# Performance work log

Hardware: AMD Instinct MI355X
Metric: run time of the kernel (lower is better)

The kernel has to match this reference:

```python
import jax, jax.numpy as jnp
import numpy as np

MARGIN = 0.3
EPS = 1e-6  # torch pairwise_distance default eps used by TripletMarginLoss


def setup_inputs() -> dict:
    key = jax.random.key(0)
    k1, k2 = jax.random.split(key)
    emb = jax.random.normal(k1, (4096, 256), dtype=jnp.float32)
    emb = emb / jnp.linalg.norm(emb, axis=1, keepdims=True)  # docstring: normalized embeddings
    labels = jax.random.randint(k2, (4096,), 0, 64, dtype=jnp.int64) if jax.config.jax_enable_x64 else jax.random.randint(k2, (4096,), 0, 64, dtype=jnp.int32)
    return {"embeddings": emb, "labels": labels}


def _triplet_mining_loss(embeddings, labels):
    B = embeddings.shape[0]
    # pairwise euclidean distances via GEMM (matches torch.cdist p=2)
    sq = jnp.sum(embeddings * embeddings, axis=1)
    d2 = sq[:, None] + sq[None, :] - 2.0 * (embeddings @ embeddings.T)
    dist = jnp.sqrt(jnp.maximum(d2, 0.0))  # [B, B]

    same = labels[:, None] == labels[None, :]
    eye = jnp.eye(B, dtype=bool)
    pos_mask = same & ~eye
    neg_mask = ~same
    valid = pos_mask.any(axis=1) & neg_mask.any(axis=1)

    # hardest positive per anchor
    ap = jnp.where(pos_mask, dist, -jnp.inf)
    hp_idx = jnp.argmax(ap, axis=1)                           # [B]
    ap_dist = jnp.take_along_axis(dist, hp_idx[:, None], 1)[:, 0]

    # semi-hard negative: ap < d_an < ap + margin; pick FIRST such index (original takes semi_hard_indices[0])
    semi = neg_mask & (dist > ap_dist[:, None]) & (dist < ap_dist[:, None] + MARGIN)
    any_semi = semi.any(axis=1)
    first_semi = jnp.argmax(semi, axis=1)                     # argmax of bool = first True
    an = jnp.where(neg_mask, dist, jnp.inf)
    hardest_neg = jnp.argmin(an, axis=1)
    neg_idx = jnp.where(any_semi, first_semi, hardest_neg)

    # triplet margin loss recomputed from embeddings (torch adds EPS inside the norm)
    pos_e = embeddings[hp_idx]
    neg_e = embeddings[neg_idx]
    d_ap = jnp.linalg.norm(embeddings - pos_e + EPS, axis=1)
    d_an = jnp.linalg.norm(embeddings - neg_e + EPS, axis=1)
    per_anchor = jnp.maximum(d_ap - d_an + MARGIN, 0.0)

    vf = valid.astype(embeddings.dtype)
    cnt = jnp.sum(vf)
    return jnp.where(cnt > 0, jnp.sum(per_anchor * vf) / jnp.maximum(cnt, 1.0), 0.0)


def reference(embeddings, labels):
    return _triplet_mining_loss(embeddings, labels)
```

## Files before the change

### kernel.cpp

```cpp
#include <hip/hip_runtime.h>
#include <math.h>

#define BN 4096
#define DIM 256
#define D4 (DIM/4)
#define MI 8
#define MT 16
#define MARGINF 0.3f
#define EPSF 1e-6f
#define SCAP 96
#define IMAX 0x7fffffff

typedef __attribute__((ext_vector_type(8))) short bf16x8;
typedef __attribute__((ext_vector_type(4))) float f32x4;

__device__ __forceinline__ float fma4(float4 a, float4 b, float c){
  return fmaf(a.x,b.x, fmaf(a.y,b.y, fmaf(a.z,b.z, fmaf(a.w,b.w, c))));
}
__device__ __forceinline__ unsigned short f2bf(float x){
  unsigned u = __float_as_uint(x);
  return (unsigned short)((u + 0x7FFFu + ((u>>16)&1u)) >> 16);
}
__device__ __forceinline__ float bf2f(unsigned short h){
  return __uint_as_float(((unsigned)h)<<16);
}

__global__ __launch_bounds__(256) void k_pre2(const float* __restrict__ E,
     unsigned short* __restrict__ EhiT, unsigned short* __restrict__ EloT,
     float* __restrict__ sq, unsigned int* __restrict__ counter){
  int t = threadIdx.x;
  int b = blockIdx.x;
  const float4* E4 = (const float4*)E;
  bf16x8* HT = (bf16x8*)EhiT;
  bf16x8* LT = (bf16x8*)EloT;
  #pragma unroll
  for (int it=0; it<8; it++){
    int g  = b*4 + (it>>1);
    int kk = (it&1)*4 + (t>>6);
    int sub = t&63, q = sub>>4, n = sub&15;
    int r = g*16 + n;
    int c = kk*4 + q;
    float4 v0 = E4[(size_t)r*64 + c*2];
    float4 v1 = E4[(size_t)r*64 + c*2 + 1];
    unsigned short h[8], lo[8];
    float vv[8] = {v0.x,v0.y,v0.z,v0.w, v1.x,v1.y,v1.z,v1.w};
    #pragma unroll
    for (int i=0;i<8;i++){ h[i]=f2bf(vv[i]); lo[i]=f2bf(vv[i]-bf2f(h[i])); }
    bf16x8 hv, lv;
    #pragma unroll
    for (int i=0;i<8;i++){ hv[i]=(short)h[i]; lv[i]=(short)lo[i]; }
    size_t d = (size_t)g*512 + (size_t)kk*64 + sub;
    HT[d] = hv; LT[d] = lv;
  }
  int row = t>>2, part = t&3;
  const float4* rp = E4 + (size_t)(b*64+row)*D4 + part*16;
  float s0=0.f, s1=0.f;
  #pragma unroll
  for (int i=0;i<16;i+=2){ s0=fma4(rp[i],rp[i],s0); s1=fma4(rp[i+1],rp[i+1],s1); }
  float s = s0+s1;
  s += __shfl_xor(s,1); s += __shfl_xor(s,2);
  if (part==0) sq[b*64+row] = s;
  if (b==0 && t==0) counter[0] = 0u;
}

__global__ __launch_bounds__(1024,4) void k_main_m(const float* __restrict__ E,
     const unsigned short* __restrict__ EhiT, const unsigned short* __restrict__ EloT,
     const int* __restrict__ labels, const float* __restrict__ sq,
     float* __restrict__ partials, unsigned int* __restrict__ counter, float* __restrict__ out){
  __shared__ int   labsS[BN];
  __shared__ float sqS[BN];
  __shared__ bf16x8 afH[512];
  __shared__ bf16x8 afL[512];
  __shared__ float rnv[16][MT]; __shared__ int rnj[16][MT]; __shared__ int rsm[16][MT];
  __shared__ float apS[MT]; __shared__ int hpS[MT]; __shared__ int posOk[MT];
  __shared__ int finNeg[MT]; __shared__ int finVal[MT];
  __shared__ float lossS[MT];
  __shared__ float rs[16], rc[16];
  __shared__ int lastFlag;
  int t=threadIdx.x, l=t&63, w=t>>6;
  int lane16 = l&15, quad = l>>4;
  int a0 = blockIdx.x * MT;
  const bf16x8* HT = (const bf16x8*)EhiT;
  const bf16x8* LT = (const bf16x8*)EloT;
  const float4* E4 = (const float4*)E;
  size_t ABase = (size_t)blockIdx.x * 512;

  ((int4*)labsS)[t]  = ((const int4*)labels)[t];
  ((float4*)sqS)[t]  = ((const float4*)sq)[t];
  if (t < 512){ afH[t] = HT[ABase + t]; afL[t] = LT[ABase + t]; }
  __syncthreads();
  float sqa[4]; int laba[4];
  #pragma unroll
  for (int r=0;r<4;r++){ sqa[r]=sqS[a0+quad*4+r]; laba[r]=labsS[a0+quad*4+r]; }

  {
    int aw = a0 + w;
    int labW = labsS[aw];
    float sqw_ = sqS[aw];
    float4 areg = E4[(size_t)aw*64 + l];
    float bv2 = -INFINITY; int bj = IMAX;
    for (int c=0; c<64; c++){
      bool m = (labsS[c*64 + l] == labW);
      unsigned long long mask = __ballot(m);
      while (mask){
        int b = __ffsll((unsigned long long)mask) - 1;
        mask &= mask - 1ull;
        int j = c*64 + b;
        if (j == aw) continue;
        float4 bjv = E4[(size_t)j*64 + l];
        float p = fma4(areg, bjv, 0.0f);
        #pragma unroll
        for (int off=32; off; off>>=1) p += __shfl_xor(p, off);
        float d2 = sqw_ + sqS[j] - 2.0f*p;
        if (d2 > bv2){ bv2 = d2; bj = j; }
      }
    }
    if (l==0){
      posOk[w] = (bj != IMAX);
      apS[w] = (bj==IMAX) ? -INFINITY : sqrtf(fmaxf(bv2, 0.0f));
      hpS[w] = (bj==IMAX) ? 0 : bj;
    }
  }
  __syncthreads();

  {
    float ap2[4], th2[4];
    #pragma unroll
    for (int r=0;r<4;r++){
      float ap = apS[quad*4+r];
      ap2[r] = ap*ap;
      float th = ap + MARGINF;
      th2[r] = th*th;
    }
    float mn[4]; int mj[4]; int sm[4];
    #pragma unroll
    for (int r=0;r<4;r++){ mn[r]=INFINITY; mj[r]=IMAX; sm[r]=IMAX; }
    #pragma unroll 1
    for (int tile=0; tile<16; tile++){
      int gb = w*16 + tile;
      size_t BBase = (size_t)gb * 512;
      f32x4 acc0={0.f,0.f,0.f,0.f}, acc1={0.f,0.f,0.f,0.f}, acc2={0.f,0.f,0.f,0.f};
      #pragma unroll 2
      for (int kk=0; kk<8; kk++){
        bf16x8 ah = afH[kk*64 + l];
        bf16x8 al = afL[kk*64 + l];
        bf16x8 bh = HT[BBase + kk*64 + l];
        bf16x8 bl = LT[BBase + kk*64 + l];
        acc0 = __builtin_amdgcn_mfma_f32_16x16x32_bf16(ah, bh, acc0, 0,0,0);
        acc1 = __builtin_amdgcn_mfma_f32_16x16x32_bf16(ah, bl, acc1, 0,0,0);
        acc2 = __builtin_amdgcn_mfma_f32_16x16x32_bf16(al, bh, acc2, 0,0,0);
      }
      int j = gb*16 + lane16;
      int lj = labsS[j]; float sqj = sqS[j];
      #pragma unroll
      for (int r=0;r<4;r++){
        float dot = acc0[r] + (acc1[r] + acc2[r]);
        float d2v = sqa[r] + sqj - 2.0f*dot;
        if (lj != laba[r]){
          if (d2v < mn[r]){ mn[r]=d2v; mj[r]=j; }
          if (d2v > ap2[r] && d2v < th2[r] && j < sm[r]) sm[r]=j;
        }
      }
    }
    #pragma unroll
    for (int r=0;r<4;r++){
      float v=mn[r]; int j=mj[r]; int s=sm[r];
      #pragma unroll
      for (int off=1; off<16; off<<=1){
        float v2=__shfl_xor(v,off); int j2=__shfl_xor(j,off); int s2=__shfl_xor(s,off);
        if (v2<v || (v2==v && j2<j)){ v=v2; j=j2; }
        s = (s2<s)?s2:s;
      }
      if (lane16==0){ rnv[w][quad*4+r]=v; rnj[w][quad*4+r]=j; rsm[w][quad*4+r]=s; }
    }
  }
  __syncthreads();
  if (t < MT){
    int a=t;
    float V=INFINITY; int J=IMAX; int S=IMAX;
    for (int q=0;q<16;q++){
      float v2=rnv[q][a]; int j2=rnj[q][a];
      if (v2<V || (v2==V && j2<J)){ V=v2; J=j2; }
      int s2=rsm[q][a]; S=(s2<S)?s2:S;
    }
    bool anyneg = (J != IMAX);
    int ng = (S != IMAX) ? S : J;
    finNeg[a] = (ng==IMAX) ? 0 : ng;
    finVal[a] = (posOk[a] && anyneg) ? 1 : 0;
  }
  __syncthreads();

  {
    int a = w;
    float sp=0.f, sn=0.f;
    int dov = finVal[a];
    if (dov){
      int hp = hpS[a], ng = finNeg[a];
      float4 av = E4[(size_t)(a0+a)*64 + l];
      float4 pv = E4[(size_t)hp*64 + l];
      float4 nv = E4[(size_t)ng*64 + l];
      float d0=av.x-pv.x+EPSF, d1=av.y-pv.y+EPSF, d2=av.z-pv.z+EPSF, d3=av.w-pv.w+EPSF;
      sp = fmaf(d0,d0, fmaf(d1,d1, fmaf(d2,d2, d3*d3)));
      float n0=av.x-nv.x+EPSF, n1=av.y-nv.y+EPSF, n2=av.z-nv.z+EPSF, n3=av.w-nv.w+EPSF;
      sn = fmaf(n0,n0, fmaf(n1,n1, fmaf(n2,n2, n3*n3)));
    }
    #pragma unroll
    for (int off=32; off; off>>=1){ sp += __shfl_xor(sp,off); sn += __shfl_xor(sn,off); }
    if (l==0) lossS[a] = dov ? fmaxf(sqrtf(sp)-sqrtf(sn)+MARGINF, 0.0f) : 0.0f;
  }
  __syncthreads();

  if (t==0){
    float lsum=0.f, lcnt=0.f;
    for (int a=0;a<MT;a++){ lsum += lossS[a]; lcnt += (float)finVal[a]; }
    partials[2*blockIdx.x]   = lsum;
    partials[2*blockIdx.x+1] = lcnt;
    __threadfence();
    unsigned int old = atomicAdd(counter, 1u);
    lastFlag = (old == gridDim.x - 1) ? 1 : 0;
  }
  __syncthreads();
  if (lastFlag){
    __threadfence();
    float s=0.f, c=0.f;
    if (t < 256){ s = partials[2*t]; c = partials[2*t+1]; }
    #pragma unroll
    for (int off=32; off; off>>=1){ s += __shfl_xor(s,off); c += __shfl_xor(c,off); }
    if (l==0){ rs[w]=s; rc[w]=c; }
    __syncthreads();
    if (t==0){
      float S=0.f, C=0.f;
      for (int q=0;q<16;q++){ S+=rs[q]; C+=rc[q]; }
      out[0] = (C>0.0f) ? S/fmaxf(C,1.0f) : 0.0f;
    }
  }
}

__global__ __launch_bounds__(256) void k_sq(const float* __restrict__ E, float* __restrict__ sq){
  int i = blockIdx.x*256 + threadIdx.x;
  if (i >= BN) return;
  const float4* r = (const float4*)E + (size_t)i*D4;
  float a0=0.f,a1=0.f,a2=0.f,a3=0.f;
  #pragma unroll
  for (int q=0;q<D4;q+=4){
    a0 = fma4(r[q],r[q],a0);   a1 = fma4(r[q+1],r[q+1],a1);
    a2 = fma4(r[q+2],r[q+2],a2); a3 = fma4(r[q+3],r[q+3],a3);
  }
  sq[i] = (a0+a1)+(a2+a3);
}

__global__ __launch_bounds__(256) void k_pos(const float* __restrict__ E, const int* __restrict__ labels,
                       const float* __restrict__ sq, float* __restrict__ apw,
                       int* __restrict__ hpw, int* __restrict__ anypw){
  __shared__ int members[1024];
  __shared__ float4 mem4[SCAP*65];
  __shared__ int cnts[16][4];
  __shared__ int offs[16][4];
  __shared__ int cntS;
  int t = threadIdx.x, lane = t&63, w = t>>6;
  int c = blockIdx.x >> 2, split = blockIdx.x & 3;
  for (int ch=0; ch<16; ch++){
    bool m = (labels[ch*256 + t] == c);
    unsigned long long mask = __ballot(m);
    if (lane==0) cnts[ch][w] = __popcll(mask);
  }
  __syncthreads();
  if (t==0){
    int run=0;
    for (int ch=0; ch<16; ch++)
      for (int q=0;q<4;q++){ offs[ch][q]=run; run+=cnts[ch][q]; }
    cntS = run;
  }
  __syncthreads();
  int cnt = cntS; if (cnt>1024) cnt=1024;
  for (int ch=0; ch<16; ch++){
    int idx = ch*256 + t;
    bool m = (labels[idx] == c);
    unsigned long long mask = __ballot(m);
    int my = __popcll(mask & ((1ull<<lane)-1ull));
    int pos = offs[ch][w] + my;
    if (m && pos < 1024) members[pos] = idx;
  }
  int S = (cnt < SCAP) ? cnt : SCAP;
  int anyp = (cnt >= 2) ? 1 : 0;
  __syncthreads();
  const float4* E4 = (const float4*)E;
  for (int idx=t; idx<S*64; idx+=256){
    int row = idx>>6, f = idx&63;
    mem4[row*65 + f] = E4[(size_t)members[row]*D4 + f];
  }
  __syncthreads();
  int esplit = split*4 + w;
  int p = lane&3, cand = lane>>2;
  int passes = (cnt+15)>>4;
  for (int mi=esplit; mi<cnt; mi+=16){
    int i = members[mi];
    float sqi = sq[i];
    float4 ai4[16];
    if (mi < S){
      #pragma unroll
      for (int m=0;m<16;m++) ai4[m] = mem4[mi*65 + p + 4*m];
    } else {
      #pragma unroll
      for (int m=0;m<16;m++) ai4[m] = E4[(size_t)i*D4 + p + 4*m];
    }
    float bv = -INFINITY; int bj = IMAX;
    for (int ps=0; ps<passes; ps++){
      int mj = ps*16 + cand;
      if (mj < cnt && mj != mi){
        int j = members[mj];
        float a0v=0.f, a1v=0.f;
        if (mj < S){
          const float4* rj = mem4 + mj*65 + p;
          #pragma unroll
          for (int m=0;m<16;m+=2){ a0v=fma4(ai4[m],rj[4*m],a0v); a1v=fma4(ai4[m+1],rj[4*(m+1)],a1v); }
        } else {
          const float4* rj = E4 + (size_t)j*D4 + p;
          #pragma unroll
          for (int m=0;m<16;m+=2){ a0v=fma4(ai4[m],rj[4*m],a0v); a1v=fma4(ai4[m+1],rj[4*(m+1)],a1v); }
        }
        float acc = a0v+a1v;
        acc += __shfl_xor(acc,1); acc += __shfl_xor(acc,2);
        float d = sqrtf(fmaxf(sqi + sq[j] - 2.0f*acc, 0.0f));
        if (p==0){ if (d > bv || (d==bv && j<bj)){ bv=d; bj=j; } }
      }
    }
    #pragma unroll
    for (int off=32; off; off>>=1){
      float v2=__shfl_xor(bv,off); int j2=__shfl_xor(bj,off);
      if (v2>bv || (v2==bv && j2<bj)){ bv=v2; bj=j2; }
    }
    if (lane==0){
      int J = (bj==IMAX) ? 0 : bj;
      apw[i]=bv; hpw[i]=J; anypw[i]=anyp;
    }
  }
}

__global__ __launch_bounds__(256,2) void k_main(const float* __restrict__ E, const int* __restrict__ labels,
     const float* __restrict__ sq, const float* __restrict__ apw, const int* __restrict__ hpw,
     const int* __restrict__ anypw, float* __restrict__ partials){
  __shared__ float4 At[MI*68 + 4];
  __shared__ float redv[4][MI]; __shared__ int redj[4][MI]; __shared__ int redsm[4][MI];
  __shared__ int finNeg[MI]; __shared__ int finVal[MI];
  __shared__ float redp[4], redn[4];
  int t=threadIdx.x, lane=t&63, w=t>>6;
  int a0 = blockIdx.x * MI;
  const float4* E4 = (const float4*)E;
  for (int idx=t; idx<MI*64; idx+=256){
    int a=idx>>6, q=idx&63, pp=q&3, mm=q>>2;
    At[a*68 + pp*17 + mm] = E4[(size_t)(a0+a)*D4 + q];
  }
  __syncthreads();
  float apv[MI], sqi[MI]; int labi[MI];
  #pragma unroll
  for (int a=0;a<MI;a++){ apv[a]=apw[a0+a]; sqi[a]=sq[a0+a]; labi[a]=labels[a0+a]; }
  float mnv[MI]; int mnj[MI]; int smj[MI];
  #pragma unroll
  for (int a=0;a<MI;a++){ mnv[a]=INFINITY; mnj[a]=0; smj[a]=IMAX; }
  int s = t>>2, p = t&3;
  for (int it=0; it<16; it++){
    int colb = it*256 + 4*s;
    const float4* __restrict__ bp = E4 + (size_t)colb*D4 + p;
    float acc[MI][4];
    #pragma unroll
    for (int a=0;a<MI;a++){
      #pragma unroll
      for (int c2=0;c2<4;c2++) acc[a][c2]=0.0f;
    }
    for (int mg=0; mg<4; mg++){
      float4 b[4][4];
      #pragma unroll
      for (int c2=0;c2<4;c2++){
        #pragma unroll
        for (int m=0;m<4;m++) b[m][c2] = bp[(size_t)c2*D4 + mg*16 + m*4];
      }
      #pragma unroll
      for (int a=0;a<MI;a++){
        float4 a4[4];
        #pragma unroll
        for (int m=0;m<4;m++) a4[m] = At[a*68 + p*17 + mg*4 + m];
        #pragma unroll
        for (int m=0;m<4;m++){
          #pragma unroll
          for (int c2=0;c2<4;c2++) acc[a][c2] = fma4(a4[m], b[m][c2], acc[a][c2]);
        }
      }
    }
    #pragma unroll
    for (int a=0;a<MI;a++){
      #pragma unroll
      for (int c2=0;c2<4;c2++){
        float v = acc[a][c2];
        v += __shfl_xor(v,1); v += __shfl_xor(v,2);
        acc[a][c2] = v;
      }
    }
    #pragma unroll
    for (int c2=0;c2<4;c2++){
      int j = colb + c2;
      int lj = labels[j]; float sqj = sq[j];
      #pragma unroll
      for (int a=0;a<MI;a++){
        float d = sqrtf(fmaxf(sqi[a]+sqj-2.0f*acc[a][c2], 0.0f));
        if (lj != labi[a]){
          if (d < mnv[a]){ mnv[a]=d; mnj[a]=j; }
          if (d > apv[a] && d < apv[a]+MARGINF && j < smj[a]) smj[a]=j;
        }
      }
    }
  }
  #pragma unroll
  for (int a=0;a<MI;a++){
    float v=mnv[a]; int j=mnj[a]; int sm=smj[a];
    #pragma unroll
    for (int off=32; off; off>>=1){
      float v2=__shfl_xor(v,off); int j2=__shfl_xor(j,off); int s2=__shfl_xor(sm,off);
      if (v2<v || (v2==v && j2<j)){ v=v2; j=j2; }
      sm = (s2<sm)?s2:sm;
    }
    if (lane==0){ redv[w][a]=v; redj[w][a]=j; redsm[w][a]=sm; }
  }
  __syncthreads();
  if (t < MI){
    int a=t;
    float V=INFINITY; int J=0; int S=IMAX; bool first=true;
    for (int q=0;q<4;q++){
      float v2=redv[q][a]; int j2=redj[q][a];
      if (first || v2<V || (v2==V && j2<J)){ V=v2; J=j2; first=false; }
      int s2=redsm[q][a]; S=(s2<S)?s2:S;
    }
    bool anyneg = (V < INFINITY);
    finNeg[a] = (S != IMAX) ? S : J;
    finVal[a] = (anypw[a0+a] != 0 && anyneg) ? 1 : 0;
  }
  __syncthreads();
  float lsum=0.0f, lcnt=0.0f;
  for (int a=0;a<MI;a++){
    if (finVal[a]){
      int hp = hpw[a0+a]; int ng = finNeg[a];
      float ai = E[(size_t)(a0+a)*DIM + t];
      float pv = E[(size_t)hp*DIM + t];
      float nv = E[(size_t)ng*DIM + t];
      float dp = ai - pv + EPSF; float dn = ai - nv + EPSF;
      float sp = dp*dp, sn = dn*dn;
      #pragma unroll
      for (int off=32; off; off>>=1){ sp += __shfl_xor(sp,off); sn += __shfl_xor(sn,off); }
      if (lane==0){ redp[w]=sp; redn[w]=sn; }
    }
    __syncthreads();
    if (finVal[a] && t==0){
      float SP=(redp[0]+redp[1])+(redp[2]+redp[3]);
      float SN=(redn[0]+redn[1])+(redn[2]+redn[3]);
      lsum += fmaxf(sqrtf(SP)-sqrtf(SN)+MARGINF, 0.0f);
      lcnt += 1.0f;
    }
    __syncthreads();
  }
  if (t==0){ partials[2*blockIdx.x]=lsum; partials[2*blockIdx.x+1]=lcnt; }
}

__global__ __launch_bounds__(256) void k_fin(const float* __restrict__ partials, float* __restrict__ out, int nb){
  __shared__ float rs[4], rc[4];
  int t=threadIdx.x, lane=t&63, w=t>>6;
  float s=0.f, c=0.f;
  for (int q=t;q<nb;q+=256){ s+=partials[2*q]; c+=partials[2*q+1]; }
  #pragma unroll
  for (int off=32; off; off>>=1){ s+=__shfl_xor(s,off); c+=__shfl_xor(c,off); }
  if (lane==0){ rs[w]=s; rc[w]=c; }
  __syncthreads();
  if (t==0){
    float S=(rs[0]+rs[1])+(rs[2]+rs[3]);
    float C=(rc[0]+rc[1])+(rc[2]+rc[3]);
    out[0] = (C>0.0f) ? S/fmaxf(C,1.0f) : 0.0f;
  }
}

extern "C" void kernel_launch(void* const* d_in, const int* in_sizes, int n_in,
                              void* d_out, int out_size, void* d_ws, size_t ws_size,
                              hipStream_t stream) {
  const float* E      = (const float*)d_in[0];
  const int*   labels = (const int*)d_in[1];
  float* out = (float*)d_out;

  float* sqw      = (float*)d_ws;
  float* apw      = sqw + BN;
  int*   hpw      = (int*)(apw + BN);
  int*   anypw    = hpw + BN;
  float* partials = (float*)(anypw + BN);
  unsigned int* counter = (unsigned int*)(partials + 1024);
  unsigned short* EhiT = (unsigned short*)((char*)d_ws + 131072);
  unsigned short* EloT = EhiT + (size_t)BN*DIM;
  bool big = ws_size >= (size_t)(131072 + 4*1024*1024);

  if (big){
    k_pre2  <<<64,    256,  0, stream>>>(E, EhiT, EloT, sqw, counter);
    k_main_m<<<BN/MT, 1024, 0, stream>>>(E, EhiT, EloT, labels, sqw, partials, counter, out);
  } else {
    k_sq  <<<BN/256, 256, 0, stream>>>(E, sqw);
    k_pos <<<256,    256, 0, stream>>>(E, labels, sqw, apw, hpw, anypw);
    k_main<<<BN/MI,  256, 0, stream>>>(E, labels, sqw, apw, hpw, anypw, partials);
    k_fin <<<1,      256, 0, stream>>>(partials, out, BN/MI);
  }
}
```

Measured before the change: 156.0 us.

## Split fused triplet kernel into positive, negative-mining and finalize stages

Replaces the single fused kernel with separate stages. A positive-mining kernel compacts same-label candidates into shared memory and computes four dot products per loop iteration. A negative-mining MFMA kernel processes 32 anchors per block over half of the candidate columns, reusing each B tile across two anchor groups, and merges the halves through 64-bit atomicMin keys. A small finalize kernel then computes the loss. This is meant to remove the serial per-anchor positive search from the MFMA kernel and raise parallelism and data reuse, at the cost of more launches, atomics and global round-trips. The positive candidate list is capped at 512 entries.

```diff
diff --git a/kernel.cpp b/kernel.cpp
--- a/kernel.cpp
+++ b/kernel.cpp
@@ -5,11 +5,11 @@
 #define DIM 256
 #define D4 (DIM/4)
 #define MI 8
-#define MT 16
 #define MARGINF 0.3f
 #define EPSF 1e-6f
 #define SCAP 96
 #define IMAX 0x7fffffff
+#define PCAP 512
 
 typedef __attribute__((ext_vector_type(8))) short bf16x8;
 typedef __attribute__((ext_vector_type(4))) float f32x4;
@@ -29,15 +29,14 @@
      unsigned short* __restrict__ EhiT, unsigned short* __restrict__ EloT,
      float* __restrict__ sq, unsigned int* __restrict__ counter){
   int t = threadIdx.x;
-  int b = blockIdx.x;
+  int g = blockIdx.x;
   const float4* E4 = (const float4*)E;
   bf16x8* HT = (bf16x8*)EhiT;
   bf16x8* LT = (bf16x8*)EloT;
   #pragma unroll
-  for (int it=0; it<8; it++){
-    int g  = b*4 + (it>>1);
-    int kk = (it&1)*4 + (t>>6);
-    int sub = t&63, q = sub>>4, n = sub&15;
+  for (int it=0; it<2; it++){
+    int idx = it*256 + t;
+    int kk = idx>>6, sub = idx&63, q = sub>>4, n = sub&15;
     int r = g*16 + n;
     int c = kk*4 + q;
     float4 v0 = E4[(size_t)r*64 + c*2];
@@ -49,172 +48,242 @@
     bf16x8 hv, lv;
     #pragma unroll
     for (int i=0;i<8;i++){ hv[i]=(short)h[i]; lv[i]=(short)lo[i]; }
-    size_t d = (size_t)g*512 + (size_t)kk*64 + sub;
+    size_t d = (size_t)g*512 + idx;
     HT[d] = hv; LT[d] = lv;
   }
-  int row = t>>2, part = t&3;
-  const float4* rp = E4 + (size_t)(b*64+row)*D4 + part*16;
-  float s0=0.f, s1=0.f;
-  #pragma unroll
-  for (int i=0;i<16;i+=2){ s0=fma4(rp[i],rp[i],s0); s1=fma4(rp[i+1],rp[i+1],s1); }
+  int row = t>>4, part = t&15;
+  const float4* rp = E4 + (size_t)(g*16+row)*64 + part*4;
+  float s0 = fma4(rp[0],rp[0],0.f);
+  float s1 = fma4(rp[1],rp[1],0.f);
+  s0 = fma4(rp[2],rp[2],s0);
+  s1 = fma4(rp[3],rp[3],s1);
   float s = s0+s1;
-  s += __shfl_xor(s,1); s += __shfl_xor(s,2);
-  if (part==0) sq[b*64+row] = s;
-  if (b==0 && t==0) counter[0] = 0u;
-}
-
-__global__ __launch_bounds__(1024,4) void k_main_m(const float* __restrict__ E,
+  s += __shfl_xor(s,1); s += __shfl_xor(s,2); s += __shfl_xor(s,4); s += __shfl_xor(s,8);
+  if (part==0) sq[g*16+row] = s;
+  if (g==0 && t==0) counter[0] = 0u;
+}
+
+__global__ __launch_bounds__(256) void k_posm(const float* __restrict__ E,
+     const int* __restrict__ labels, const float* __restrict__ sq,
+     float* __restrict__ apw, int* __restrict__ hpw,
+     unsigned long long* __restrict__ negKey, unsigned int* __restrict__ semiJ){
+  __shared__ __align__(16) int   labsS[BN];
+  __shared__ __align__(16) float sqS[BN];
+  __shared__ int mem[4][PCAP+4];
+  int t=threadIdx.x, l=t&63, w=t>>6;
+  #pragma unroll
+  for (int i=0;i<4;i++){
+    ((int4*)labsS)[i*256+t]   = ((const int4*)labels)[i*256+t];
+    ((float4*)sqS)[i*256+t]   = ((const float4*)sq)[i*256+t];
+  }
+  __syncthreads();
+  int aw = blockIdx.x*4 + w;
+  int labW = labsS[aw];
+  float sqw_ = sqS[aw];
+  const float4* E4 = (const float4*)E;
+  float4 areg = E4[(size_t)aw*64 + l];
+  int cnt = 0;
+  for (int c=0;c<64;c++){
+    int j = c*64 + l;
+    bool m = (labsS[j]==labW) && (j != aw);
+    unsigned long long mask = __ballot(m);
+    if (m){
+      int pos = cnt + __popcll(mask & ((1ull<<l)-1ull));
+      if (pos < PCAP) mem[w][pos] = j;
+    }
+    cnt += __popcll(mask);
+  }
+  if (cnt > PCAP) cnt = PCAP;
+  if (l < 4) mem[w][cnt + l] = aw;
+  float bv2 = -INFINITY; int bj = IMAX;
+  for (int base=0; base<cnt; base+=4){
+    int j0=mem[w][base+0], j1=mem[w][base+1], j2=mem[w][base+2], j3=mem[w][base+3];
+    float4 r0=E4[(size_t)j0*64+l];
+    float4 r1=E4[(size_t)j1*64+l];
+    float4 r2=E4[(size_t)j2*64+l];
+    float4 r3=E4[(size_t)j3*64+l];
+    float p0=fma4(areg,r0,0.f), p1=fma4(areg,r1,0.f);
+    float p2=fma4(areg,r2,0.f), p3=fma4(areg,r3,0.f);
+    #pragma unroll
+    for (int off=32; off; off>>=1){
+      p0 += __shfl_xor(p0,off); p1 += __shfl_xor(p1,off);
+      p2 += __shfl_xor(p2,off); p3 += __shfl_xor(p3,off);
+    }
+    float d0 = sqw_ + sqS[j0] - 2.0f*p0;
+    float d1 = sqw_ + sqS[j1] - 2.0f*p1;
+    float d2 = sqw_ + sqS[j2] - 2.0f*p2;
+    float d3 = sqw_ + sqS[j3] - 2.0f*p3;
+    if (d0 > bv2){ bv2=d0; bj=j0; }
+    if (base+1<cnt && d1 > bv2){ bv2=d1; bj=j1; }
+    if (base+2<cnt && d2 > bv2){ bv2=d2; bj=j2; }
+    if (base+3<cnt && d3 > bv2){ bv2=d3; bj=j3; }
+  }
+  if (l==0){
+    apw[aw] = (bj==IMAX) ? -INFINITY : sqrtf(fmaxf(bv2, 0.0f));
+    hpw[aw] = (bj==IMAX) ? 0 : bj;
+    negKey[aw] = ~0ull;
+    semiJ[aw]  = 0xFFFFFFFFu;
+  }
+}
+
+__global__ __launch_bounds__(1024,4) void k_negm(
      const unsigned short* __restrict__ EhiT, const unsigned short* __restrict__ EloT,
      const int* __restrict__ labels, const float* __restrict__ sq,
-     float* __restrict__ partials, unsigned int* __restrict__ counter, float* __restrict__ out){
-  __shared__ int   labsS[BN];
-  __shared__ float sqS[BN];
-  __shared__ bf16x8 afH[512];
-  __shared__ bf16x8 afL[512];
-  __shared__ float rnv[16][MT]; __shared__ int rnj[16][MT]; __shared__ int rsm[16][MT];
-  __shared__ float apS[MT]; __shared__ int hpS[MT]; __shared__ int posOk[MT];
-  __shared__ int finNeg[MT]; __shared__ int finVal[MT];
-  __shared__ float lossS[MT];
-  __shared__ float rs[16], rc[16];
-  __shared__ int lastFlag;
+     const float* __restrict__ apw,
+     unsigned long long* __restrict__ negKey, unsigned int* __restrict__ semiJ){
+  __shared__ bf16x8 afH[1024];
+  __shared__ bf16x8 afL[1024];
+  __shared__ __align__(16) int   labsH[2048];
+  __shared__ __align__(16) float sqH[2048];
+  __shared__ float rnv[16][32]; __shared__ int rnj[16][32]; __shared__ int rsm[16][32];
   int t=threadIdx.x, l=t&63, w=t>>6;
   int lane16 = l&15, quad = l>>4;
-  int a0 = blockIdx.x * MT;
+  int q8   = blockIdx.x & 7;
+  int half = q8 >> 2;
+  int grp  = (blockIdx.x >> 3)*4 + (q8 & 3);
+  int a0 = grp*32;
+  int hbase = half*2048;
   const bf16x8* HT = (const bf16x8*)EhiT;
   const bf16x8* LT = (const bf16x8*)EloT;
-  const float4* E4 = (const float4*)E;
-  size_t ABase = (size_t)blockIdx.x * 512;
-
-  ((int4*)labsS)[t]  = ((const int4*)labels)[t];
-  ((float4*)sqS)[t]  = ((const float4*)sq)[t];
-  if (t < 512){ afH[t] = HT[ABase + t]; afL[t] = LT[ABase + t]; }
-  __syncthreads();
-  float sqa[4]; int laba[4];
-  #pragma unroll
-  for (int r=0;r<4;r++){ sqa[r]=sqS[a0+quad*4+r]; laba[r]=labsS[a0+quad*4+r]; }
-
-  {
-    int aw = a0 + w;
-    int labW = labsS[aw];
-    float sqw_ = sqS[aw];
-    float4 areg = E4[(size_t)aw*64 + l];
-    float bv2 = -INFINITY; int bj = IMAX;
-    for (int c=0; c<64; c++){
-      bool m = (labsS[c*64 + l] == labW);
-      unsigned long long mask = __ballot(m);
-      while (mask){
-        int b = __ffsll((unsigned long long)mask) - 1;
-        mask &= mask - 1ull;
-        int j = c*64 + b;
-        if (j == aw) continue;
-        float4 bjv = E4[(size_t)j*64 + l];
-        float p = fma4(areg, bjv, 0.0f);
-        #pragma unroll
-        for (int off=32; off; off>>=1) p += __shfl_xor(p, off);
-        float d2 = sqw_ + sqS[j] - 2.0f*p;
-        if (d2 > bv2){ bv2 = d2; bj = j; }
-      }
-    }
-    if (l==0){
-      posOk[w] = (bj != IMAX);
-      apS[w] = (bj==IMAX) ? -INFINITY : sqrtf(fmaxf(bv2, 0.0f));
-      hpS[w] = (bj==IMAX) ? 0 : bj;
-    }
-  }
-  __syncthreads();
-
-  {
-    float ap2[4], th2[4];
-    #pragma unroll
-    for (int r=0;r<4;r++){
-      float ap = apS[quad*4+r];
-      ap2[r] = ap*ap;
+  afH[t] = HT[(size_t)grp*1024 + t];
+  afL[t] = LT[(size_t)grp*1024 + t];
+  { int2   lv = ((const int2*)(labels + hbase))[t];
+    labsH[2*t] = lv.x; labsH[2*t+1] = lv.y;
+    float2 sv = ((const float2*)(sq + hbase))[t];
+    sqH[2*t] = sv.x; sqH[2*t+1] = sv.y; }
+  float sqa[2][4]; int laba[2][4]; float ap2[2][4]; float th2[2][4];
+  #pragma unroll
+  for (int g=0; g<2; g++){
+    #pragma unroll
+    for (int r=0; r<4; r++){
+      int ag = a0 + g*16 + quad*4 + r;
+      sqa[g][r] = sq[ag]; laba[g][r] = labels[ag];
+      float ap = apw[ag];
+      ap2[g][r] = ap*ap;
       float th = ap + MARGINF;
-      th2[r] = th*th;
-    }
-    float mn[4]; int mj[4]; int sm[4];
-    #pragma unroll
-    for (int r=0;r<4;r++){ mn[r]=INFINITY; mj[r]=IMAX; sm[r]=IMAX; }
-    #pragma unroll 1
-    for (int tile=0; tile<16; tile++){
-      int gb = w*16 + tile;
-      size_t BBase = (size_t)gb * 512;
-      f32x4 acc0={0.f,0.f,0.f,0.f}, acc1={0.f,0.f,0.f,0.f}, acc2={0.f,0.f,0.f,0.f};
-      #pragma unroll 2
-      for (int kk=0; kk<8; kk++){
-        bf16x8 ah = afH[kk*64 + l];
-        bf16x8 al = afL[kk*64 + l];
-        bf16x8 bh = HT[BBase + kk*64 + l];
-        bf16x8 bl = LT[BBase + kk*64 + l];
-        acc0 = __builtin_amdgcn_mfma_f32_16x16x32_bf16(ah, bh, acc0, 0,0,0);
-        acc1 = __builtin_amdgcn_mfma_f32_16x16x32_bf16(ah, bl, acc1, 0,0,0);
-        acc2 = __builtin_amdgcn_mfma_f32_16x16x32_bf16(al, bh, acc2, 0,0,0);
-      }
-      int j = gb*16 + lane16;
-      int lj = labsS[j]; float sqj = sqS[j];
-      #pragma unroll
-      for (int r=0;r<4;r++){
-        float dot = acc0[r] + (acc1[r] + acc2[r]);
-        float d2v = sqa[r] + sqj - 2.0f*dot;
-        if (lj != laba[r]){
-          if (d2v < mn[r]){ mn[r]=d2v; mj[r]=j; }
-          if (d2v > ap2[r] && d2v < th2[r] && j < sm[r]) sm[r]=j;
-        }
-      }
-    }
-    #pragma unroll
-    for (int r=0;r<4;r++){
-      float v=mn[r]; int j=mj[r]; int s=sm[r];
+      th2[g][r] = th*th;
+    }
+  }
+  __syncthreads();
+  float mn[2][4]; int mj[2][4]; int sm[2][4];
+  #pragma unroll
+  for (int g=0; g<2; g++)
+    #pragma unroll
+    for (int r=0; r<4; r++){ mn[g][r]=INFINITY; mj[g][r]=IMAX; sm[g][r]=IMAX; }
+  #pragma unroll 1
+  for (int tile=0; tile<8; tile++){
+    int gl = w*8 + tile;
+    size_t BBase = (size_t)(half*128 + gl) * 512;
+    f32x4 acc00={0.f,0.f,0.f,0.f}, acc01=acc00, acc02=acc00;
+    f32x4 acc10=acc00, acc11=acc00, acc12=acc00;
+    #pragma unroll 2
+    for (int kk=0; kk<8; kk++){
+      bf16x8 bh  = HT[BBase + kk*64 + l];
+      bf16x8 bl  = LT[BBase + kk*64 + l];
+      bf16x8 ah0 = afH[kk*64 + l];
+      bf16x8 al0 = afL[kk*64 + l];
+      bf16x8 ah1 = afH[512 + kk*64 + l];
+      bf16x8 al1 = afL[512 + kk*64 + l];
+      acc00 = __builtin_amdgcn_mfma_f32_16x16x32_bf16(ah0, bh, acc00, 0,0,0);
+      acc01 = __builtin_amdgcn_mfma_f32_16x16x32_bf16(ah0, bl, acc01, 0,0,0);
+      acc02 = __builtin_amdgcn_mfma_f32_16x16x32_bf16(al0, bh, acc02, 0,0,0);
+      acc10 = __builtin_amdgcn_mfma_f32_16x16x32_bf16(ah1, bh, acc10, 0,0,0);
+      acc11 = __builtin_amdgcn_mfma_f32_16x16x32_bf16(ah1, bl, acc11, 0,0,0);
+      acc12 = __builtin_amdgcn_mfma_f32_16x16x32_bf16(al1, bh, acc12, 0,0,0);
+    }
+    int jloc = gl*16 + lane16;
+    int lj = labsH[jloc]; float sqj = sqH[jloc];
+    int jglob = hbase + jloc;
+    #pragma unroll
+    for (int r=0; r<4; r++){
+      float dot0 = acc00[r] + (acc01[r] + acc02[r]);
+      float d20  = sqa[0][r] + sqj - 2.0f*dot0;
+      if (lj != laba[0][r]){
+        if (d20 < mn[0][r]){ mn[0][r]=d20; mj[0][r]=jglob; }
+        if (d20 > ap2[0][r] && d20 < th2[0][r] && jglob < sm[0][r]) sm[0][r]=jglob;
+      }
+      float dot1 = acc10[r] + (acc11[r] + acc12[r]);
+      float d21  = sqa[1][r] + sqj - 2.0f*dot1;
+      if (lj != laba[1][r]){
+        if (d21 < mn[1][r]){ mn[1][r]=d21; mj[1][r]=jglob; }
+        if (d21 > ap2[1][r] && d21 < th2[1][r] && jglob < sm[1][r]) sm[1][r]=jglob;
+      }
+    }
+  }
+  #pragma unroll
+  for (int g=0; g<2; g++){
+    #pragma unroll
+    for (int r=0; r<4; r++){
+      float v=mn[g][r]; int j=mj[g][r]; int s=sm[g][r];
       #pragma unroll
       for (int off=1; off<16; off<<=1){
         float v2=__shfl_xor(v,off); int j2=__shfl_xor(j,off); int s2=__shfl_xor(s,off);
         if (v2<v || (v2==v && j2<j)){ v=v2; j=j2; }
         s = (s2<s)?s2:s;
       }
-      if (lane16==0){ rnv[w][quad*4+r]=v; rnj[w][quad*4+r]=j; rsm[w][quad*4+r]=s; }
-    }
-  }
-  __syncthreads();
-  if (t < MT){
-    int a=t;
+      if (lane16==0){
+        int ai = g*16 + quad*4 + r;
+        rnv[w][ai]=v; rnj[w][ai]=j; rsm[w][ai]=s;
+      }
+    }
+  }
+  __syncthreads();
+  if (t < 32){
     float V=INFINITY; int J=IMAX; int S=IMAX;
-    for (int q=0;q<16;q++){
-      float v2=rnv[q][a]; int j2=rnj[q][a];
+    for (int q=0; q<16; q++){
+      float v2=rnv[q][t]; int j2=rnj[q][t];
       if (v2<V || (v2==V && j2<J)){ V=v2; J=j2; }
-      int s2=rsm[q][a]; S=(s2<S)?s2:S;
-    }
-    bool anyneg = (J != IMAX);
-    int ng = (S != IMAX) ? S : J;
-    finNeg[a] = (ng==IMAX) ? 0 : ng;
-    finVal[a] = (posOk[a] && anyneg) ? 1 : 0;
-  }
-  __syncthreads();
-
-  {
-    int a = w;
-    float sp=0.f, sn=0.f;
-    int dov = finVal[a];
+      int s2=rsm[q][t]; S=(s2<S)?s2:S;
+    }
+    unsigned u = __float_as_uint(V);
+    unsigned key = (u & 0x80000000u) ? ~u : (u | 0x80000000u);
+    unsigned long long k64 = (((unsigned long long)key)<<32) | (unsigned)J;
+    atomicMin(&negKey[a0+t], k64);
+    if (S != IMAX) atomicMin(&semiJ[a0+t], (unsigned)S);
+  }
+}
+
+__global__ __launch_bounds__(256) void k_fin2(const float* __restrict__ E,
+     const float* __restrict__ apw, const int* __restrict__ hpw,
+     const unsigned long long* __restrict__ negKey, const unsigned int* __restrict__ semiJ,
+     float* __restrict__ partials, unsigned int* __restrict__ counter,
+     float* __restrict__ out){
+  __shared__ float lsumS[4], lcntS[4];
+  __shared__ float rs[4], rc[4];
+  __shared__ int lastFlag;
+  int t=threadIdx.x, l=t&63, w=t>>6;
+  const float4* E4 = (const float4*)E;
+  float lsum=0.f, lcnt=0.f;
+  #pragma unroll 1
+  for (int i=0;i<4;i++){
+    int a = blockIdx.x*16 + w*4 + i;
+    unsigned long long k64 = negKey[a];
+    unsigned Jn = (unsigned)(k64 & 0xFFFFFFFFull);
+    unsigned Sn = semiJ[a];
+    bool anyneg = (Jn != (unsigned)IMAX);
+    int ng = (Sn != 0xFFFFFFFFu) ? (int)Sn : (int)Jn;
+    float ap = apw[a];
+    bool dov = (ap != -INFINITY) && anyneg;
     if (dov){
-      int hp = hpS[a], ng = finNeg[a];
-      float4 av = E4[(size_t)(a0+a)*64 + l];
+      int hp = hpw[a];
+      float4 av = E4[(size_t)a*64 + l];
       float4 pv = E4[(size_t)hp*64 + l];
       float4 nv = E4[(size_t)ng*64 + l];
       float d0=av.x-pv.x+EPSF, d1=av.y-pv.y+EPSF, d2=av.z-pv.z+EPSF, d3=av.w-pv.w+EPSF;
-      sp = fmaf(d0,d0, fmaf(d1,d1, fmaf(d2,d2, d3*d3)));
+      float sp = fmaf(d0,d0, fmaf(d1,d1, fmaf(d2,d2, d3*d3)));
       float n0=av.x-nv.x+EPSF, n1=av.y-nv.y+EPSF, n2=av.z-nv.z+EPSF, n3=av.w-nv.w+EPSF;
-      sn = fmaf(n0,n0, fmaf(n1,n1, fmaf(n2,n2, n3*n3)));
-    }
-    #pragma unroll
-    for (int off=32; off; off>>=1){ sp += __shfl_xor(sp,off); sn += __shfl_xor(sn,off); }
-    if (l==0) lossS[a] = dov ? fmaxf(sqrtf(sp)-sqrtf(sn)+MARGINF, 0.0f) : 0.0f;
-  }
-  __syncthreads();
-
+      float sn = fmaf(n0,n0, fmaf(n1,n1, fmaf(n2,n2, n3*n3)));
+      #pragma unroll
+      for (int off=32; off; off>>=1){ sp += __shfl_xor(sp,off); sn += __shfl_xor(sn,off); }
+      lsum += fmaxf(sqrtf(sp)-sqrtf(sn)+MARGINF, 0.0f);
+      lcnt += 1.0f;
+    }
+  }
+  if (l==0){ lsumS[w]=lsum; lcntS[w]=lcnt; }
+  __syncthreads();
   if (t==0){
-    float lsum=0.f, lcnt=0.f;
-    for (int a=0;a<MT;a++){ lsum += lossS[a]; lcnt += (float)finVal[a]; }
-    partials[2*blockIdx.x]   = lsum;
-    partials[2*blockIdx.x+1] = lcnt;
+    partials[2*blockIdx.x]   = (lsumS[0]+lsumS[1])+(lsumS[2]+lsumS[3]);
+    partials[2*blockIdx.x+1] = (lcntS[0]+lcntS[1])+(lcntS[2]+lcntS[3]);
     __threadfence();
     unsigned int old = atomicAdd(counter, 1u);
     lastFlag = (old == gridDim.x - 1) ? 1 : 0;
@@ -222,15 +291,14 @@
   __syncthreads();
   if (lastFlag){
     __threadfence();
-    float s=0.f, c=0.f;
-    if (t < 256){ s = partials[2*t]; c = partials[2*t+1]; }
+    float s = partials[2*t], c = partials[2*t+1];
     #pragma unroll
     for (int off=32; off; off>>=1){ s += __shfl_xor(s,off); c += __shfl_xor(c,off); }
     if (l==0){ rs[w]=s; rc[w]=c; }
     __syncthreads();
     if (t==0){
-      float S=0.f, C=0.f;
-      for (int q=0;q<16;q++){ S+=rs[q]; C+=rc[q]; }
+      float S=(rs[0]+rs[1])+(rs[2]+rs[3]);
+      float C=(rc[0]+rc[1])+(rc[2]+rc[3]);
       out[0] = (C>0.0f) ? S/fmaxf(C,1.0f) : 0.0f;
     }
   }
@@ -489,13 +557,17 @@
   int*   anypw    = hpw + BN;
   float* partials = (float*)(anypw + BN);
   unsigned int* counter = (unsigned int*)(partials + 1024);
+  unsigned long long* negKey = (unsigned long long*)((char*)d_ws + 72*1024);
+  unsigned int*       semiJ  = (unsigned int*)((char*)d_ws + 104*1024);
   unsigned short* EhiT = (unsigned short*)((char*)d_ws + 131072);
   unsigned short* EloT = EhiT + (size_t)BN*DIM;
   bool big = ws_size >= (size_t)(131072 + 4*1024*1024);
 
   if (big){
-    k_pre2  <<<64,    256,  0, stream>>>(E, EhiT, EloT, sqw, counter);
-    k_main_m<<<BN/MT, 1024, 0, stream>>>(E, EhiT, EloT, labels, sqw, partials, counter, out);
+    k_pre2<<<256,  256,  0, stream>>>(E, EhiT, EloT, sqw, counter);
+    k_posm<<<1024, 256,  0, stream>>>(E, labels, sqw, apw, hpw, negKey, semiJ);
+    k_negm<<<256,  1024, 0, stream>>>(EhiT, EloT, labels, sqw, apw, negKey, semiJ);
+    k_fin2<<<256,  256,  0, stream>>>(E, apw, hpw, negKey, semiJ, partials, counter, out);
   } else {
     k_sq  <<<BN/256, 256, 0, stream>>>(E, sqw);
     k_pos <<<256,    256, 0, stream>>>(E, labels, sqw, apw, hpw, anypw);
```

Result: faster. 152.0 us (-2.6%).
